# Optimization experiments

Hardware: AMD Instinct MI355X
Metric: run time of the kernel (lower is better)

Reference implementation:

```python
import jax, jax.numpy as jnp
import numpy as np

# ---- static problem sizes (full batches: cum[b] = b * max_num) ----
B = 256          # graphs per batch
MAXN, MAXE, MAXC = 128, 256, 64   # max nodes / edges / 2-cells per graph
H = 256          # embed_dim == hidden
L = 4            # num GCNCConv layers
OUT = 10         # out_size
P_N, P_E = 131072, 98304          # up-adjacency pair counts (dim 0, dim 1)
Q_E, Q_C = 131072, 65536          # boundary incidence counts (dim 1, dim 2)


def setup_inputs() -> dict:
    key = jax.random.key(0)
    ks = jax.random.split(key, 24)
    s = 1.0 / np.sqrt(H)
    inp = {}
    # flat cochain features [total_entities, H]
    inp['x_n'] = jax.random.normal(ks[0], (B * MAXN, H), jnp.float32)
    inp['x_e'] = jax.random.normal(ks[1], (B * MAXE, H), jnp.float32)
    inp['x_c'] = jax.random.normal(ks[2], (B * MAXC, H), jnp.float32)
    # node-level up adjacency (pairs of nodes sharing an edge coboundary)
    inp['n_up_b'] = jax.random.randint(ks[3], (P_N,), 0, B, jnp.int32)
    inp['n_up_i'] = jax.random.randint(ks[4], (P_N,), 0, MAXN, jnp.int32)
    inp['n_up_j'] = jax.random.randint(ks[5], (P_N,), 0, MAXN, jnp.int32)
    inp['n_up_e'] = jax.random.randint(ks[6], (P_N,), 0, MAXE, jnp.int32)
    # edge-level up adjacency (pairs of edges sharing a cell coboundary)
    inp['e_up_b'] = jax.random.randint(ks[7], (P_E,), 0, B, jnp.int32)
    inp['e_up_i'] = jax.random.randint(ks[8], (P_E,), 0, MAXE, jnp.int32)
    inp['e_up_j'] = jax.random.randint(ks[9], (P_E,), 0, MAXE, jnp.int32)
    inp['e_up_c'] = jax.random.randint(ks[10], (P_E,), 0, MAXC, jnp.int32)
    # boundary incidence: edges -> nodes, cells -> edges
    inp['eb_b'] = jax.random.randint(ks[11], (Q_E,), 0, B, jnp.int32)
    inp['eb_i'] = jax.random.randint(ks[12], (Q_E,), 0, MAXE, jnp.int32)
    inp['eb_j'] = jax.random.randint(ks[13], (Q_E,), 0, MAXN, jnp.int32)
    inp['cb_b'] = jax.random.randint(ks[14], (Q_C,), 0, B, jnp.int32)
    inp['cb_i'] = jax.random.randint(ks[15], (Q_C,), 0, MAXC, jnp.int32)
    inp['cb_j'] = jax.random.randint(ks[16], (Q_C,), 0, MAXE, jnp.int32)
    # learned parameters
    inp['Wself'] = jax.random.normal(ks[17], (L, 3, H, H), jnp.float32) * s
    inp['bself'] = jnp.zeros((L, 3, H), jnp.float32)
    inp['Wupx'] = jax.random.normal(ks[18], (L, 2, H, H), jnp.float32) * s
    inp['Wupa'] = jax.random.normal(ks[19], (L, 2, H, H), jnp.float32) * s
    inp['Wb'] = jax.random.normal(ks[20], (L, 2, H, H), jnp.float32) * s
    inp['Wp'] = jax.random.normal(ks[21], (H, H), jnp.float32) * s
    inp['Wp_ref'] = jax.random.normal(ks[22], (H, H), jnp.float32) * s
    inp['bp'] = jnp.zeros((H,), jnp.float32)
    k2 = jax.random.split(ks[23], 4)
    inp['W1'] = jax.random.normal(k2[0], (3, H, 2 * H), jnp.float32) * s
    inp['b1'] = jnp.zeros((3, 2 * H), jnp.float32)
    inp['W2'] = jax.random.normal(k2[1], (2 * H, OUT), jnp.float32) * s
    inp['b2'] = jnp.zeros((OUT,), jnp.float32)
    return inp


def reference(x_n, x_e, x_c, n_up_b, n_up_i, n_up_j, n_up_e,
              e_up_b, e_up_i, e_up_j, e_up_c, eb_b, eb_i, eb_j,
              cb_b, cb_i, cb_j, Wself, bself, Wupx, Wupa, Wb,
              Wp, Wp_ref, bp, W1, b1, W2, b2):
    relu = jax.nn.relu
    # dense per-batch boundary adjacencies (scatter-set, as in init_data_to_dense_gcnc)
    b_adj_e = jnp.zeros((B, MAXE, MAXN), jnp.float32).at[eb_b, eb_i, eb_j].set(1.0)
    b_adj_c = jnp.zeros((B, MAXC, MAXE), jnp.float32).at[cb_b, cb_i, cb_j].set(1.0)
    # flat gather/scatter indices: cum[b] = b * max_num (full batches)
    n_i = n_up_b * MAXN + n_up_i
    n_j = n_up_b * MAXN + n_up_j
    n_a = n_up_b * MAXE + n_up_e   # up_attr_idx into edge features
    e_i = e_up_b * MAXE + e_up_i
    e_j = e_up_b * MAXE + e_up_j
    e_a = e_up_b * MAXC + e_up_c   # up_attr_idx into cell features
    xs = [x_n, x_e, x_c]
    refs = xs  # init features used by pool_weight
    for l in range(L):
        xn, xe, xc = xs
        # up messages: msg = relu(W x_j + W' up_attr), scatter-sum to receiver
        up_n = jax.ops.segment_sum(
            relu(xn[n_j] @ Wupx[l, 0] + xe[n_a] @ Wupa[l, 0]),
            n_i, num_segments=B * MAXN)
        up_e = jax.ops.segment_sum(
            relu(xe[e_j] @ Wupx[l, 1] + xc[e_a] @ Wupa[l, 1]),
            e_i, num_segments=B * MAXE)
        # boundary messages: dense masked matmul with incidence matrices
        bd_e = jnp.einsum('ben,bnh->beh', b_adj_e,
                          xn.reshape(B, MAXN, H)).reshape(B * MAXE, H) @ Wb[l, 0]
        bd_c = jnp.einsum('bce,beh->bch', b_adj_c,
                          xe.reshape(B, MAXE, H)).reshape(B * MAXC, H) @ Wb[l, 1]
        xs = [relu(xn @ Wself[l, 0] + bself[l, 0] + up_n),
              relu(xe @ Wself[l, 1] + bself[l, 1] + up_e + bd_e),
              relu(xc @ Wself[l, 2] + bself[l, 2] + bd_c)]
    # pool weights (gating vs. init features) + sum readout per dimension
    maxs = (MAXN, MAXE, MAXC)
    pooled = []
    for i in range(3):
        w = jax.nn.sigmoid(xs[i] @ Wp + refs[i] @ Wp_ref + bp)
        pooled.append((w * xs[i]).reshape(B, maxs[i], H).sum(axis=1))  # [B,H]
    h = sum(relu(pooled[i] @ W1[i] + b1[i]) for i in range(3))  # final_readout='sum'
    return h @ W2 + b2  # [B, OUT]
```

## Files before the change

kernel.cpp:

```cpp
#include <hip/hip_runtime.h>
#include <cstdint>
#include <cstddef>

typedef unsigned short u16;
typedef __bf16 bf16x8 __attribute__((ext_vector_type(8)));
typedef float f32x4 __attribute__((ext_vector_type(4)));
typedef unsigned short u16x8 __attribute__((ext_vector_type(8)));

#define NB   256
#define MAXN 128
#define MAXE 256
#define MAXC 64
#define HD   256
#define NLAYER 4
#define PN 131072
#define PE 98304
#define QE 131072
#define QC 65536
#define MN (NB*MAXN)
#define ME (NB*MAXE)
#define MC (NB*MAXC)

#define SEG_N  0
#define SEG_E  (MN)
#define SEG_EB (MN + ME)
#define SEG_CB (MN + 2*ME)
#define HTOT   (MN + 2*ME + MC)
#define UPTOT  (PN + PE)

__device__ __forceinline__ float bf2f(u16 u){
  union{unsigned int i; float f;} x; x.i = ((unsigned int)u) << 16; return x.f;
}
__device__ __forceinline__ u16 f2bf(float f){
  union{float f; unsigned int i;} x; x.f = f;
  unsigned int r = x.i + 0x7fffu + ((x.i >> 16) & 1u);
  return (u16)(r >> 16);
}
__device__ __forceinline__ f32x4 MFMA(bf16x8 a, bf16x8 b, f32x4 c){
  return __builtin_amdgcn_mfma_f32_16x16x32_bf16(a, b, c, 0, 0, 0);
}
__device__ __forceinline__ void gl_lds16(const u16* g, u16* l){
  __builtin_amdgcn_global_load_lds(
      (const __attribute__((address_space(1))) unsigned int*)g,
      (__attribute__((address_space(3))) unsigned int*)l, 16, 0, 0);
}

__global__ void detect_dtype(const u16* __restrict__ x, int* __restrict__ flag){
  if(threadIdx.x == 0 && blockIdx.x == 0){
    int cnt = 0;
    for(int i = 0; i < 64; i++){
      int e = (x[i] >> 7) & 0xFF;
      if(e >= 118 && e <= 136) cnt++;
    }
    *flag = (cnt >= 50) ? 1 : 0;
  }
}

__global__ __launch_bounds__(256) void conv_bf(const void* __restrict__ src, u16* __restrict__ dst,
                                               long n, const int* __restrict__ flag){
  long i = ((long)blockIdx.x * 256 + threadIdx.x) * 8;
  if(i >= n) return;
  const int isbf = *flag;
  if(i + 8 <= n){
    if(isbf){
      *reinterpret_cast<u16x8*>(dst + i) = *reinterpret_cast<const u16x8*>((const u16*)src + i);
    }else{
      const float* s = (const float*)src + i;
      float4 a = *reinterpret_cast<const float4*>(s);
      float4 b = *reinterpret_cast<const float4*>(s + 4);
      u16x8 o;
      o[0]=f2bf(a.x); o[1]=f2bf(a.y); o[2]=f2bf(a.z); o[3]=f2bf(a.w);
      o[4]=f2bf(b.x); o[5]=f2bf(b.y); o[6]=f2bf(b.z); o[7]=f2bf(b.w);
      *reinterpret_cast<u16x8*>(dst + i) = o;
    }
  }else{
    for(long e = i; e < n; e++)
      dst[e] = isbf ? ((const u16*)src)[e] : f2bf(((const float*)src)[e]);
  }
}

__global__ __launch_bounds__(256) void zero_f4(float* __restrict__ p, long n4){
  long i = (long)blockIdx.x * blockDim.x + threadIdx.x;
  if(i >= n4) return;
  float4 z = {0.f, 0.f, 0.f, 0.f};
  *reinterpret_cast<float4*>(p + i * 4) = z;
}

__global__ void wt_transpose(const void* __restrict__ src, u16* __restrict__ dst,
                             const int* __restrict__ flag){
  __shared__ u16 t[16][17];
  int m = blockIdx.z;
  int n0 = blockIdx.x * 16, k0 = blockIdx.y * 16;
  size_t sidx = (size_t)m * 65536 + (size_t)(k0 + threadIdx.y) * 256 + n0 + threadIdx.x;
  u16 v = (*flag) ? ((const u16*)src)[sidx] : f2bf(((const float*)src)[sidx]);
  t[threadIdx.y][threadIdx.x] = v;
  __syncthreads();
  dst[(size_t)m * 65536 + (size_t)(n0 + threadIdx.y) * 256 + (k0 + threadIdx.x)] =
      t[threadIdx.x][threadIdx.y];
}

__global__ void dedup_kernel(const int* __restrict__ bb, const int* __restrict__ bi,
                             const int* __restrict__ bj, unsigned int* __restrict__ mask,
                             unsigned char* __restrict__ valid, int Q, int maxI, int maxJ){
  int q = blockIdx.x * blockDim.x + threadIdx.x;
  if(q >= Q) return;
  int s = (bb[q] * maxI + bi[q]) * maxJ + bj[q];
  unsigned int bit = 1u << (s & 31);
  unsigned int old = atomicOr(&mask[s >> 5], bit);
  valid[q] = (old & bit) ? 0 : 1;
}

__global__ __launch_bounds__(256) void hist_up(const int* __restrict__ pb, const int* __restrict__ pi,
                                               int maxI, int segBase, int* __restrict__ hist, int P){
  int p = blockIdx.x * 256 + threadIdx.x;
  if(p >= P) return;
  atomicAdd(&hist[segBase + pb[p] * maxI + pi[p]], 1);
}
__global__ __launch_bounds__(256) void hist_bd(const int* __restrict__ bb, const int* __restrict__ bi,
                                               const unsigned char* __restrict__ valid,
                                               int maxI, int segBase, int* __restrict__ hist, int Q){
  int q = blockIdx.x * 256 + threadIdx.x;
  if(q >= Q || !valid[q]) return;
  atomicAdd(&hist[segBase + bb[q] * maxI + bi[q]], 1);
}

__global__ __launch_bounds__(256) void scan1(const int* __restrict__ hist, int* __restrict__ bsum){
  __shared__ int s[256];
  int t = threadIdx.x;
  long base = (long)blockIdx.x * 1024 + t * 4;
  int4 v = *reinterpret_cast<const int4*>(hist + base);
  s[t] = v.x + v.y + v.z + v.w;
  __syncthreads();
  for(int st = 128; st > 0; st >>= 1){
    if(t < st) s[t] += s[t + st];
    __syncthreads();
  }
  if(t == 0) bsum[blockIdx.x] = s[0];
}
__global__ __launch_bounds__(256) void scan2(int* __restrict__ bsum, int nb){
  __shared__ int s[256];
  int t = threadIdx.x;
  int v = (t < nb) ? bsum[t] : 0;
  s[t] = v;
  __syncthreads();
  for(int st = 1; st < 256; st <<= 1){
    int u = (t >= st) ? s[t - st] : 0;
    __syncthreads();
    s[t] += u;
    __syncthreads();
  }
  if(t < nb) bsum[t] = s[t] - v;
}
__global__ __launch_bounds__(256) void scan3(const int* __restrict__ hist, const int* __restrict__ bsum,
                                             int* __restrict__ off, int* __restrict__ cur){
  __shared__ int s[256];
  int t = threadIdx.x;
  long base = (long)blockIdx.x * 1024 + t * 4;
  int4 v = *reinterpret_cast<const int4*>(hist + base);
  int sum = v.x + v.y + v.z + v.w;
  s[t] = sum;
  __syncthreads();
  for(int st = 1; st < 256; st <<= 1){
    int u = (t >= st) ? s[t - st] : 0;
    __syncthreads();
    s[t] += u;
    __syncthreads();
  }
  int excl = s[t] - sum + bsum[blockIdx.x];
  int4 o;
  o.x = excl; o.y = o.x + v.x; o.z = o.y + v.y; o.w = o.z + v.z;
  *reinterpret_cast<int4*>(off + base) = o;
  *reinterpret_cast<int4*>(cur + base) = o;
}

__global__ __launch_bounds__(256) void fill_up(const int* __restrict__ pb, const int* __restrict__ pi,
    const int* __restrict__ pj, const int* __restrict__ pa, int maxI, int maxA, int segBase,
    int* __restrict__ cur, int2* __restrict__ csrUp, int P){
  int p = blockIdx.x * 256 + threadIdx.x;
  if(p >= P) return;
  int b = pb[p];
  int pos = atomicAdd(&cur[segBase + b * maxI + pi[p]], 1);
  int2 e; e.x = b * maxI + pj[p]; e.y = b * maxA + pa[p];
  csrUp[pos] = e;
}
__global__ __launch_bounds__(256) void fill_bd(const int* __restrict__ bb, const int* __restrict__ bi,
    const int* __restrict__ bj, const unsigned char* __restrict__ valid, int maxI, int maxJ,
    int segBase, int* __restrict__ cur, int* __restrict__ csrBd, int Q){
  int q = blockIdx.x * 256 + threadIdx.x;
  if(q >= Q || !valid[q]) return;
  int b = bb[q];
  int pos = atomicAdd(&cur[segBase + b * maxI + bi[q]], 1);
  csrBd[pos - UPTOT] = b * maxJ + bj[q];
}

template<int HAS_UP, int HAS_BD>
__global__ __launch_bounds__(256) void gather_k(
    const u16* __restrict__ Y, const u16* __restrict__ Z, const u16* __restrict__ BD,
    const int2* __restrict__ csrUp, const int* __restrict__ csrBd,
    const int* __restrict__ off, const int* __restrict__ deg,
    int upBase, int bdBase, u16* __restrict__ ACC, int rowLo){
  const int nb = gridDim.x;
  int bx = blockIdx.x;
  if((nb & 7) == 0) bx = (bx & 7) * (nb >> 3) + (bx >> 3);
  const int row = rowLo + bx * 4 + (threadIdx.x >> 6);
  const int lane = threadIdx.x & 63;
  const int c = lane * 4;
  float a0 = 0.f, a1 = 0.f, a2 = 0.f, a3 = 0.f;
  if(HAS_UP){
    int s = off[upBase + row];
    int d = deg[upBase + row];
    for(int k = 0; k < d; k++){
      int2 e = csrUp[s + k];
      const ushort4 y = *reinterpret_cast<const ushort4*>(Y + (size_t)e.x * 256 + c);
      const ushort4 z = *reinterpret_cast<const ushort4*>(Z + (size_t)e.y * 256 + c);
      a0 += fmaxf(bf2f(y.x) + bf2f(z.x), 0.f);
      a1 += fmaxf(bf2f(y.y) + bf2f(z.y), 0.f);
      a2 += fmaxf(bf2f(y.z) + bf2f(z.z), 0.f);
      a3 += fmaxf(bf2f(y.w) + bf2f(z.w), 0.f);
    }
  }
  if(HAS_BD){
    int s = off[bdBase + row] - UPTOT;
    int d = deg[bdBase + row];
    for(int k = 0; k < d; k++){
      int j = csrBd[s + k];
      const ushort4 x = *reinterpret_cast<const ushort4*>(BD + (size_t)j * 256 + c);
      a0 += bf2f(x.x); a1 += bf2f(x.y); a2 += bf2f(x.z); a3 += bf2f(x.w);
    }
  }
  ushort4 o; o.x = f2bf(a0); o.y = f2bf(a1); o.z = f2bf(a2); o.w = f2bf(a3);
  *reinterpret_cast<ushort4*>(ACC + (size_t)(row - rowLo) * 256 + c) = o;
}

template<int MODE>
__global__ __launch_bounds__(512) void gemm_b(const u16* A, const u16* __restrict__ WT,
                                              u16* C, const u16* __restrict__ ACC,
                                              const u16* __restrict__ bias,
                                              const u16* A2, const u16* __restrict__ WT2){
  __shared__ u16 lA[2][128 * 64];
  __shared__ u16 lB[2][256 * 64];
  const int t = threadIdx.x;
  const int lane = t & 63, wv = t >> 6;
  const int wm = wv >> 2, wn = wv & 3;
  const int r = lane & 15, q = lane >> 4;
  const int rsw = r & 7;
  const size_t m0 = (size_t)blockIdx.x * 128;
  const int lrow = lane >> 3, lchk = lane & 7;
  const int csw = lchk ^ lrow;

  f32x4 acc[4][4];
#pragma unroll
  for(int i = 0; i < 4; i++)
#pragma unroll
    for(int j = 0; j < 4; j++) acc[i][j] = {0.f, 0.f, 0.f, 0.f};

  const int NT = (MODE == 3) ? 8 : 4;

  auto stage = [&](int tt, int buf){
    const u16* Ap = (MODE == 3 && tt >= 4) ? A2 : A;
    const u16* Wp = (MODE == 3 && tt >= 4) ? WT2 : WT;
    const int k0 = (tt & 3) * 64;
#pragma unroll
    for(int i = 0; i < 2; i++){
      const int row = i * 64 + wv * 8 + lrow;
      gl_lds16(Ap + (m0 + row) * 256 + k0 + csw * 8, &lA[buf][(i * 64 + wv * 8) * 64]);
    }
#pragma unroll
    for(int j = 0; j < 4; j++){
      const int n = j * 64 + wv * 8 + lrow;
      gl_lds16(Wp + (size_t)n * 256 + k0 + csw * 8, &lB[buf][(j * 64 + wv * 8) * 64]);
    }
  };

  stage(0, 0);
  __syncthreads();

#pragma unroll
  for(int tt = 0; tt < NT; tt++){
    const int cur = tt & 1;
    if(tt + 1 < NT) stage(tt + 1, cur ^ 1);
#pragma unroll
    for(int ks = 0; ks < 2; ks++){
      bf16x8 af[4], bfr[4];
#pragma unroll
      for(int i = 0; i < 4; i++)
        af[i] = *reinterpret_cast<const bf16x8*>(
            &lA[cur][(wm * 64 + i * 16 + r) * 64 + (((ks * 4 + q) ^ rsw) * 8)]);
#pragma unroll
      for(int j = 0; j < 4; j++)
        bfr[j] = *reinterpret_cast<const bf16x8*>(
            &lB[cur][(wn * 64 + j * 16 + r) * 64 + (((ks * 4 + q) ^ rsw) * 8)]);
#pragma unroll
      for(int i = 0; i < 4; i++)
#pragma unroll
        for(int j = 0; j < 4; j++) acc[i][j] = MFMA(af[i], bfr[j], acc[i][j]);
    }
    __syncthreads();
  }

#pragma unroll
  for(int i = 0; i < 4; i++){
    const size_t row0 = m0 + wm * 64 + i * 16 + q * 4;
#pragma unroll
    for(int j = 0; j < 4; j++){
      const int col = wn * 64 + j * 16 + r;
#pragma unroll
      for(int reg = 0; reg < 4; reg++){
        const size_t idx = (row0 + reg) * 256 + col;
        float x = acc[i][j][reg];
        if(MODE == 2) x = fmaxf(x + bf2f(ACC[idx]) + bf2f(bias[col]), 0.f);
        C[idx] = f2bf(x);
      }
    }
  }
}

__global__ __launch_bounds__(256) void pool_reduce(const u16* __restrict__ G, const u16* __restrict__ bpv,
    const u16* __restrict__ X, float* __restrict__ pooled, int maxR, int rowsPerBlk){
  int b = blockIdx.x, h = threadIdx.x;
  int r0 = blockIdx.y * rowsPerBlk;
  float bias = bf2f(bpv[h]);
  float acc = 0.f;
  for(int r = r0; r < r0 + rowsPerBlk; r++){
    size_t o = ((size_t)b * maxR + r) * 256 + h;
    float t = bf2f(G[o]) + bias;
    float w = 1.f / (1.f + __expf(-t));
    acc += w * bf2f(X[o]);
  }
  atomicAdd(&pooled[b * 256 + h], acc);
}

__global__ __launch_bounds__(512) void readout1(const float* __restrict__ pooled, const u16* __restrict__ W1,
                                                const u16* __restrict__ b1, float* __restrict__ hbuf){
  __shared__ float p[3][256];
  int b = blockIdx.x, o = threadIdx.x;
  if(o < 256){
    p[0][o] = pooled[(size_t)b * 256 + o];
    p[1][o] = pooled[(size_t)NB * 256 + (size_t)b * 256 + o];
    p[2][o] = pooled[(size_t)2 * NB * 256 + (size_t)b * 256 + o];
  }
  __syncthreads();
  float s = 0.f;
#pragma unroll
  for(int i = 0; i < 3; i++){
    float a = bf2f(b1[i * 512 + o]);
    for(int k = 0; k < 256; k++) a += p[i][k] * bf2f(W1[(size_t)(i * 256 + k) * 512 + o]);
    s += fmaxf(a, 0.f);
  }
  hbuf[(size_t)b * 512 + o] = s;
}

__global__ __launch_bounds__(64) void readout2(const float* __restrict__ hbuf, const u16* __restrict__ W2,
                                               const u16* __restrict__ b2, void* __restrict__ out,
                                               const int* __restrict__ flag){
  int b = blockIdx.x, o = threadIdx.x;
  if(o >= 10) return;
  float a = bf2f(b2[o]);
  for(int k = 0; k < 512; k++) a += hbuf[(size_t)b * 512 + k] * bf2f(W2[k * 10 + o]);
  if(*flag) ((u16*)out)[b * 10 + o] = f2bf(a);
  else      ((float*)out)[b * 10 + o] = a;
}

extern "C" void kernel_launch(void* const* d_in, const int* in_sizes, int n_in,
                              void* d_out, int out_size, void* d_ws, size_t ws_size,
                              hipStream_t stream){
  const void* x_n = d_in[0];
  const void* x_e = d_in[1];
  const void* x_c = d_in[2];
  const int* n_up_b = (const int*)d_in[3];
  const int* n_up_i = (const int*)d_in[4];
  const int* n_up_j = (const int*)d_in[5];
  const int* n_up_e = (const int*)d_in[6];
  const int* e_up_b = (const int*)d_in[7];
  const int* e_up_i = (const int*)d_in[8];
  const int* e_up_j = (const int*)d_in[9];
  const int* e_up_c = (const int*)d_in[10];
  const int* eb_b = (const int*)d_in[11];
  const int* eb_i = (const int*)d_in[12];
  const int* eb_j = (const int*)d_in[13];
  const int* cb_b = (const int*)d_in[14];
  const int* cb_i = (const int*)d_in[15];
  const int* cb_j = (const int*)d_in[16];

  char* base = (char*)d_ws; size_t off0 = 0;
  auto alloc = [&](size_t n)->char*{ char* p = base + off0; off0 = (off0 + n + 255) & ~(size_t)255; return p; };
  u16* xn = (u16*)alloc((size_t)MN * HD * 2);
  u16* xe = (u16*)alloc((size_t)ME * HD * 2);
  u16* xc = (u16*)alloc((size_t)MC * HD * 2);
  u16* BIG1 = (u16*)alloc((size_t)ME * HD * 2);
  u16* SMa  = (u16*)alloc((size_t)MN * HD * 2);
  u16* SMb  = (u16*)alloc((size_t)MN * HD * 2);
  u16* ACC  = (u16*)alloc((size_t)16384 * HD * 4);
  u16* wt = (u16*)alloc((size_t)38 * 65536 * 2);
  unsigned int* mask_e = (unsigned int*)alloc((size_t)NB * MAXE * MAXN / 8);
  unsigned int* mask_c = (unsigned int*)alloc((size_t)NB * MAXC * MAXE / 8);
  unsigned char* valid_e = (unsigned char*)alloc(QE);
  unsigned char* valid_c = (unsigned char*)alloc(QC);
  float* pooled = (float*)alloc((size_t)3 * NB * HD * 4);
  float* hbuf   = (float*)alloc((size_t)NB * 512 * 4);
  int* flag     = (int*)alloc(256);
  int2* csrUp   = (int2*)alloc((size_t)UPTOT * 8);
  int* csrBd    = (int*)alloc((size_t)(QE + QC) * 4);
  int* hist     = (int*)alloc((size_t)HTOT * 4);
  int* offA     = (int*)alloc((size_t)HTOT * 4);
  int* bsum     = (int*)alloc(1024);
  int* cur      = (int*)pooled;

  u16* wtSelf = wt;
  u16* wtUpx  = wt + (size_t)12 * 65536;
  u16* wtUpa  = wt + (size_t)20 * 65536;
  u16* wtB    = wt + (size_t)28 * 65536;
  u16* wtP    = wt + (size_t)36 * 65536;
  u16* wtPref = wt + (size_t)37 * 65536;

  u16* W1c = (u16*)mask_e;
  u16* b1c = W1c + 393216;
  u16* W2c = b1c + 1536;
  u16* b2c = W2c + 5120;
  u16* bsc = b2c + 16;
  u16* bpc = bsc + 3072;

  auto convN = [&](const void* s, u16* d, long n){
    long blk = (n + 8*256 - 1) / (8*256);
    conv_bf<<<(int)blk, 256, 0, stream>>>(s, d, n, flag);
  };

  detect_dtype<<<1, 64, 0, stream>>>((const u16*)x_n, flag);
  zero_f4<<<(65536 + 255)/256, 256, 0, stream>>>((float*)mask_e, 65536);
  zero_f4<<<(32768 + 255)/256, 256, 0, stream>>>((float*)mask_c, 32768);
  dedup_kernel<<<QE/256, 256, 0, stream>>>(eb_b, eb_i, eb_j, mask_e, valid_e, QE, MAXE, MAXN);
  dedup_kernel<<<QC/256, 256, 0, stream>>>(cb_b, cb_i, cb_j, mask_c, valid_c, QC, MAXC, MAXE);

  wt_transpose<<<dim3(16,16,12), dim3(16,16), 0, stream>>>(d_in[17], wtSelf, flag);
  wt_transpose<<<dim3(16,16,8),  dim3(16,16), 0, stream>>>(d_in[19], wtUpx,  flag);
  wt_transpose<<<dim3(16,16,8),  dim3(16,16), 0, stream>>>(d_in[20], wtUpa,  flag);
  wt_transpose<<<dim3(16,16,8),  dim3(16,16), 0, stream>>>(d_in[21], wtB,    flag);
  wt_transpose<<<dim3(16,16,1),  dim3(16,16), 0, stream>>>(d_in[22], wtP,    flag);
  wt_transpose<<<dim3(16,16,1),  dim3(16,16), 0, stream>>>(d_in[23], wtPref, flag);
  convN(x_n, xn, (long)MN * HD);
  convN(x_e, xe, (long)ME * HD);
  convN(x_c, xc, (long)MC * HD);
  convN(d_in[18], bsc, 3072);
  convN(d_in[24], bpc, 256);
  convN(d_in[25], W1c, 393216);
  convN(d_in[26], b1c, 1536);
  convN(d_in[27], W2c, 5120);
  convN(d_in[28], b2c, 10);

  zero_f4<<<(HTOT/4 + 255)/256, 256, 0, stream>>>((float*)hist, HTOT/4);
  hist_up<<<PN/256, 256, 0, stream>>>(n_up_b, n_up_i, MAXN, SEG_N,  hist, PN);
  hist_up<<<PE/256, 256, 0, stream>>>(e_up_b, e_up_i, MAXE, SEG_E,  hist, PE);
  hist_bd<<<QE/256, 256, 0, stream>>>(eb_b, eb_i, valid_e, MAXE, SEG_EB, hist, QE);
  hist_bd<<<QC/256, 256, 0, stream>>>(cb_b, cb_i, valid_c, MAXC, SEG_CB, hist, QC);
  scan1<<<HTOT/1024, 256, 0, stream>>>(hist, bsum);
  scan2<<<1, 256, 0, stream>>>(bsum, HTOT/1024);
  scan3<<<HTOT/1024, 256, 0, stream>>>(hist, bsum, offA, cur);
  fill_up<<<PN/256, 256, 0, stream>>>(n_up_b, n_up_i, n_up_j, n_up_e, MAXN, MAXE, SEG_N, cur, csrUp, PN);
  fill_up<<<PE/256, 256, 0, stream>>>(e_up_b, e_up_i, e_up_j, e_up_c, MAXE, MAXC, SEG_E, cur, csrUp, PE);
  fill_bd<<<QE/256, 256, 0, stream>>>(eb_b, eb_i, eb_j, valid_e, MAXE, MAXN, SEG_EB, cur, csrBd, QE);
  fill_bd<<<QC/256, 256, 0, stream>>>(cb_b, cb_i, cb_j, valid_c, MAXC, MAXE, SEG_CB, cur, csrBd, QC);

  for(int l = 0; l < NLAYER; l++){
    const u16* Wupx0 = wtUpx + (size_t)(l*2+0) * 65536;
    const u16* Wupx1 = wtUpx + (size_t)(l*2+1) * 65536;
    const u16* Wupa0 = wtUpa + (size_t)(l*2+0) * 65536;
    const u16* Wupa1 = wtUpa + (size_t)(l*2+1) * 65536;
    const u16* Wb0   = wtB   + (size_t)(l*2+0) * 65536;
    const u16* Wb1   = wtB   + (size_t)(l*2+1) * 65536;
    const u16* Ws0   = wtSelf + (size_t)(l*3+0) * 65536;
    const u16* Ws1   = wtSelf + (size_t)(l*3+1) * 65536;
    const u16* Ws2   = wtSelf + (size_t)(l*3+2) * 65536;
    const u16* bs0 = bsc + (size_t)(l*3+0) * HD;
    const u16* bs1 = bsc + (size_t)(l*3+1) * HD;
    const u16* bs2 = bsc + (size_t)(l*3+2) * HD;

    gemm_b<0><<<MN/128, 512, 0, stream>>>(xn, Wupx0, SMa, nullptr, nullptr, nullptr, nullptr);
    gemm_b<0><<<ME/128, 512, 0, stream>>>(xe, Wupa0, BIG1, nullptr, nullptr, nullptr, nullptr);
    gemm_b<0><<<MN/128, 512, 0, stream>>>(xn, Wb0, SMb, nullptr, nullptr, nullptr, nullptr);
    for(int h = 0; h < 2; h++){
      int lo = h * (MN/2);
      gather_k<1,0><<<(MN/2)/4, 256, 0, stream>>>(SMa, BIG1, nullptr, csrUp, csrBd,
                                                  offA, hist, SEG_N, 0, ACC, lo);
      gemm_b<2><<<(MN/2)/128, 512, 0, stream>>>(xn + (size_t)lo * HD, Ws0,
                                                xn + (size_t)lo * HD, ACC, bs0, nullptr, nullptr);
    }

    gemm_b<0><<<MC/128, 512, 0, stream>>>(xc, Wupa1, SMa, nullptr, nullptr, nullptr, nullptr);
    gemm_b<0><<<ME/128, 512, 0, stream>>>(xe, Wb1, BIG1, nullptr, nullptr, nullptr, nullptr);
    gather_k<0,1><<<MC/4, 256, 0, stream>>>(nullptr, nullptr, BIG1, csrUp, csrBd,
                                            offA, hist, 0, SEG_CB, ACC, 0);
    gemm_b<2><<<MC/128, 512, 0, stream>>>(xc, Ws2, xc, ACC, bs2, nullptr, nullptr);

    gemm_b<0><<<ME/128, 512, 0, stream>>>(xe, Wupx1, BIG1, nullptr, nullptr, nullptr, nullptr);
    for(int h = 0; h < 2; h++){
      int lo = h * (ME/2);
      gather_k<1,1><<<(ME/2)/4, 256, 0, stream>>>(BIG1, SMa, SMb, csrUp, csrBd,
                                                  offA, hist, SEG_E, SEG_EB, ACC, lo);
      gemm_b<2><<<(ME/2)/128, 512, 0, stream>>>(xe + (size_t)lo * HD, Ws1,
                                                xe + (size_t)lo * HD, ACC, bs1, nullptr, nullptr);
    }
  }

  u16* REF = SMa;
  {
    long np4 = (long)3 * NB * HD / 4;
    zero_f4<<<(int)((np4 + 255)/256), 256, 0, stream>>>(pooled, np4);
  }
  convN(x_n, REF, (long)MN * HD);
  gemm_b<3><<<MN/128, 512, 0, stream>>>(xn, wtP, BIG1, nullptr, nullptr, REF, wtPref);
  pool_reduce<<<dim3(NB,2), 256, 0, stream>>>(BIG1, bpc, xn, pooled, MAXN, MAXN/2);

  convN(x_e, REF, (long)ME * HD);
  gemm_b<3><<<ME/128, 512, 0, stream>>>(xe, wtP, BIG1, nullptr, nullptr, REF, wtPref);
  pool_reduce<<<dim3(NB,4), 256, 0, stream>>>(BIG1, bpc, xe, pooled + (size_t)NB*HD, MAXE, MAXE/4);

  convN(x_c, REF, (long)MC * HD);
  gemm_b<3><<<MC/128, 512, 0, stream>>>(xc, wtP, BIG1, nullptr, nullptr, REF, wtPref);
  pool_reduce<<<dim3(NB,1), 256, 0, stream>>>(BIG1, bpc, xc, pooled + (size_t)2*NB*HD, MAXC, MAXC);

  readout1<<<NB, 512, 0, stream>>>(pooled, W1c, b1c, hbuf);
  readout2<<<NB, 64, 0, stream>>>(hbuf, W2c, b2c, d_out, flag);
}
```

Baseline: 1.537 ms.

## Triple-buffer GEMM tile loads with explicit waitcnt and transpose readout W1

The GEMM main loop moves from double to triple buffering in LDS. Loads are issued up to three k-tiles ahead and gated with explicit s_waitcnt vmcnt counts and raw barriers instead of __syncthreads, so more global-to-LDS traffic overlaps with MFMA work. LDS use rises to about 288KB-equivalent per block worth of u16 (3×(128+256)×64×2 bytes ≈ 147KB), which may cut occupancy or exceed limits. Separately, the readout weight W1 is transposed once so each thread reads contiguous 16-byte vectors instead of strided scalars.

```diff
diff --git a/kernel.cpp b/kernel.cpp
--- a/kernel.cpp
+++ b/kernel.cpp
@@ -96,6 +96,17 @@
   t[threadIdx.y][threadIdx.x] = v;
   __syncthreads();
   dst[(size_t)m * 65536 + (size_t)(n0 + threadIdx.y) * 256 + (k0 + threadIdx.x)] =
+      t[threadIdx.x][threadIdx.y];
+}
+
+__global__ void w1_transpose(const u16* __restrict__ src, u16* __restrict__ dst){
+  __shared__ u16 t[16][17];
+  int i = blockIdx.z;
+  int o0 = blockIdx.x * 16, k0 = blockIdx.y * 16;
+  t[threadIdx.y][threadIdx.x] =
+      src[(size_t)i * 131072 + (size_t)(k0 + threadIdx.y) * 512 + o0 + threadIdx.x];
+  __syncthreads();
+  dst[(size_t)i * 131072 + (size_t)(o0 + threadIdx.y) * 256 + (k0 + threadIdx.x)] =
       t[threadIdx.x][threadIdx.y];
 }
 
@@ -237,8 +248,8 @@
                                               u16* C, const u16* __restrict__ ACC,
                                               const u16* __restrict__ bias,
                                               const u16* A2, const u16* __restrict__ WT2){
-  __shared__ u16 lA[2][128 * 64];
-  __shared__ u16 lB[2][256 * 64];
+  __shared__ u16 lA[3][128 * 64];
+  __shared__ u16 lB[3][256 * 64];
   const int t = threadIdx.x;
   const int lane = t & 63, wv = t >> 6;
   const int wm = wv >> 2, wn = wv & 3;
@@ -273,12 +284,17 @@
   };
 
   stage(0, 0);
-  __syncthreads();
+  stage(1, 1);
+  stage(2, 2);
 
 #pragma unroll
   for(int tt = 0; tt < NT; tt++){
-    const int cur = tt & 1;
-    if(tt + 1 < NT) stage(tt + 1, cur ^ 1);
+    const int cur = tt % 3;
+    const int rem = NT - 1 - tt;
+    if(rem >= 2)      asm volatile("s_waitcnt vmcnt(12)" ::: "memory");
+    else if(rem == 1) asm volatile("s_waitcnt vmcnt(6)" ::: "memory");
+    else              asm volatile("s_waitcnt vmcnt(0)" ::: "memory");
+    __builtin_amdgcn_s_barrier();
 #pragma unroll
     for(int ks = 0; ks < 2; ks++){
       bf16x8 af[4], bfr[4];
@@ -295,7 +311,8 @@
 #pragma unroll
         for(int j = 0; j < 4; j++) acc[i][j] = MFMA(af[i], bfr[j], acc[i][j]);
     }
-    __syncthreads();
+    __builtin_amdgcn_s_barrier();
+    if(tt + 3 < NT) stage(tt + 3, cur);
   }
 
 #pragma unroll
@@ -330,7 +347,7 @@
   atomicAdd(&pooled[b * 256 + h], acc);
 }
 
-__global__ __launch_bounds__(512) void readout1(const float* __restrict__ pooled, const u16* __restrict__ W1,
+__global__ __launch_bounds__(512) void readout1(const float* __restrict__ pooled, const u16* __restrict__ W1t,
                                                 const u16* __restrict__ b1, float* __restrict__ hbuf){
   __shared__ float p[3][256];
   int b = blockIdx.x, o = threadIdx.x;
@@ -344,7 +361,14 @@
 #pragma unroll
   for(int i = 0; i < 3; i++){
     float a = bf2f(b1[i * 512 + o]);
-    for(int k = 0; k < 256; k++) a += p[i][k] * bf2f(W1[(size_t)(i * 256 + k) * 512 + o]);
+    const u16* w = W1t + (size_t)i * 131072 + (size_t)o * 256;
+#pragma unroll 4
+    for(int k8 = 0; k8 < 32; k8++){
+      u16x8 wv = *reinterpret_cast<const u16x8*>(w + k8 * 8);
+      const float* pp = &p[i][k8 * 8];
+      a += pp[0]*bf2f(wv[0]) + pp[1]*bf2f(wv[1]) + pp[2]*bf2f(wv[2]) + pp[3]*bf2f(wv[3])
+         + pp[4]*bf2f(wv[4]) + pp[5]*bf2f(wv[5]) + pp[6]*bf2f(wv[6]) + pp[7]*bf2f(wv[7]);
+    }
     s += fmaxf(a, 0.f);
   }
   hbuf[(size_t)b * 512 + o] = s;
@@ -404,6 +428,7 @@
   int* hist     = (int*)alloc((size_t)HTOT * 4);
   int* offA     = (int*)alloc((size_t)HTOT * 4);
   int* bsum     = (int*)alloc(1024);
+  u16* W1t      = (u16*)alloc((size_t)3 * 512 * 256 * 2);
   int* cur      = (int*)pooled;
 
   u16* wtSelf = wt;
@@ -446,6 +471,7 @@
   convN(d_in[26], b1c, 1536);
   convN(d_in[27], W2c, 5120);
   convN(d_in[28], b2c, 10);
+  w1_transpose<<<dim3(32,16,3), dim3(16,16), 0, stream>>>(W1c, W1t);
 
   zero_f4<<<(HTOT/4 + 255)/256, 256, 0, stream>>>((float*)hist, HTOT/4);
   hist_up<<<PN/256, 256, 0, stream>>>(n_up_b, n_up_i, MAXN, SEG_N,  hist, PN);
@@ -518,6 +544,6 @@
   gemm_b<3><<<MC/128, 512, 0, stream>>>(xc, wtP, BIG1, nullptr, nullptr, REF, wtPref);
   pool_reduce<<<dim3(NB,1), 256, 0, stream>>>(BIG1, bpc, xc, pooled + (size_t)2*NB*HD, MAXC, MAXC);
 
-  readout1<<<NB, 512, 0, stream>>>(pooled, W1c, b1c, hbuf);
+  readout1<<<NB, 512, 0, stream>>>(pooled, W1t, b1c, hbuf);
   readout2<<<NB, 64, 0, stream>>>(hbuf, W2c, b2c, d_out, flag);
 }
```

Measured after the change: 1.509 ms. Within noise of the previous version (-1.8%).

## Shrink GEMM tiles, deepen prefetch pipeline, and move readout1 to MFMA

Applied to the files above, without the earlier changes.

The main GEMM now uses a 64-row tile with 256 threads and issues the next two K-stages ahead. It waits with explicit vmcnt counters and raw barriers, and raises wave priority during the MFMA section. This doubles the grid size, which helps occupancy, and overlaps loads more deeply with compute. The scalar readout1 kernel is replaced by an MFMA-based kernel that takes a bf16 copy of the pooled features and a pre-transposed W1, which removes a slow per-thread dot-product loop. The trade-offs are that B tiles are reloaded more often per output row, and pooled features are rounded to bf16 before the readout.

```diff
diff --git a/kernel.cpp b/kernel.cpp
--- a/kernel.cpp
+++ b/kernel.cpp
@@ -79,6 +79,17 @@
   }
 }
 
+__global__ __launch_bounds__(256) void conv_f2b(const float* __restrict__ s, u16* __restrict__ d, long n){
+  long i = ((long)blockIdx.x * 256 + threadIdx.x) * 8;
+  if(i >= n) return;
+  float4 a = *reinterpret_cast<const float4*>(s + i);
+  float4 b = *reinterpret_cast<const float4*>(s + i + 4);
+  u16x8 o;
+  o[0]=f2bf(a.x); o[1]=f2bf(a.y); o[2]=f2bf(a.z); o[3]=f2bf(a.w);
+  o[4]=f2bf(b.x); o[5]=f2bf(b.y); o[6]=f2bf(b.z); o[7]=f2bf(b.w);
+  *reinterpret_cast<u16x8*>(d + i) = o;
+}
+
 __global__ __launch_bounds__(256) void zero_f4(float* __restrict__ p, long n4){
   long i = (long)blockIdx.x * blockDim.x + threadIdx.x;
   if(i >= n4) return;
@@ -96,6 +107,17 @@
   t[threadIdx.y][threadIdx.x] = v;
   __syncthreads();
   dst[(size_t)m * 65536 + (size_t)(n0 + threadIdx.y) * 256 + (k0 + threadIdx.x)] =
+      t[threadIdx.x][threadIdx.y];
+}
+
+__global__ void w1_transpose(const u16* __restrict__ src, u16* __restrict__ dst){
+  __shared__ u16 t[16][17];
+  int i = blockIdx.z;
+  int o0 = blockIdx.x * 16, k0 = blockIdx.y * 16;
+  t[threadIdx.y][threadIdx.x] =
+      src[(size_t)i * 131072 + (size_t)(k0 + threadIdx.y) * 512 + o0 + threadIdx.x];
+  __syncthreads();
+  dst[(size_t)i * 131072 + (size_t)(o0 + threadIdx.y) * 256 + (k0 + threadIdx.x)] =
       t[threadIdx.x][threadIdx.y];
 }
 
@@ -233,18 +255,18 @@
 }
 
 template<int MODE>
-__global__ __launch_bounds__(512) void gemm_b(const u16* A, const u16* __restrict__ WT,
+__global__ __launch_bounds__(256) void gemm_b(const u16* A, const u16* __restrict__ WT,
                                               u16* C, const u16* __restrict__ ACC,
                                               const u16* __restrict__ bias,
                                               const u16* A2, const u16* __restrict__ WT2){
-  __shared__ u16 lA[2][128 * 64];
+  __shared__ u16 lA[2][64 * 64];
   __shared__ u16 lB[2][256 * 64];
   const int t = threadIdx.x;
   const int lane = t & 63, wv = t >> 6;
-  const int wm = wv >> 2, wn = wv & 3;
+  const int wn = wv;
   const int r = lane & 15, q = lane >> 4;
   const int rsw = r & 7;
-  const size_t m0 = (size_t)blockIdx.x * 128;
+  const size_t m0 = (size_t)blockIdx.x * 64;
   const int lrow = lane >> 3, lchk = lane & 7;
   const int csw = lchk ^ lrow;
 
@@ -262,30 +284,33 @@
     const int k0 = (tt & 3) * 64;
 #pragma unroll
     for(int i = 0; i < 2; i++){
-      const int row = i * 64 + wv * 8 + lrow;
-      gl_lds16(Ap + (m0 + row) * 256 + k0 + csw * 8, &lA[buf][(i * 64 + wv * 8) * 64]);
-    }
-#pragma unroll
-    for(int j = 0; j < 4; j++){
-      const int n = j * 64 + wv * 8 + lrow;
-      gl_lds16(Wp + (size_t)n * 256 + k0 + csw * 8, &lB[buf][(j * 64 + wv * 8) * 64]);
+      const int row = wv * 16 + i * 8 + lrow;
+      gl_lds16(Ap + (m0 + row) * 256 + k0 + csw * 8, &lA[buf][(wv * 16 + i * 8) * 64]);
+    }
+#pragma unroll
+    for(int j = 0; j < 8; j++){
+      const int n = wv * 64 + j * 8 + lrow;
+      gl_lds16(Wp + (size_t)n * 256 + k0 + csw * 8, &lB[buf][(wv * 64 + j * 8) * 64]);
     }
   };
 
   stage(0, 0);
-  __syncthreads();
+  stage(1, 1);
 
 #pragma unroll
   for(int tt = 0; tt < NT; tt++){
     const int cur = tt & 1;
-    if(tt + 1 < NT) stage(tt + 1, cur ^ 1);
+    if(tt < NT - 1) asm volatile("s_waitcnt vmcnt(10)" ::: "memory");
+    else            asm volatile("s_waitcnt vmcnt(0)" ::: "memory");
+    __builtin_amdgcn_s_barrier();
+    __builtin_amdgcn_s_setprio(1);
 #pragma unroll
     for(int ks = 0; ks < 2; ks++){
       bf16x8 af[4], bfr[4];
 #pragma unroll
       for(int i = 0; i < 4; i++)
         af[i] = *reinterpret_cast<const bf16x8*>(
-            &lA[cur][(wm * 64 + i * 16 + r) * 64 + (((ks * 4 + q) ^ rsw) * 8)]);
+            &lA[cur][(i * 16 + r) * 64 + (((ks * 4 + q) ^ rsw) * 8)]);
 #pragma unroll
       for(int j = 0; j < 4; j++)
         bfr[j] = *reinterpret_cast<const bf16x8*>(
@@ -295,12 +320,14 @@
 #pragma unroll
         for(int j = 0; j < 4; j++) acc[i][j] = MFMA(af[i], bfr[j], acc[i][j]);
     }
-    __syncthreads();
+    __builtin_amdgcn_s_setprio(0);
+    __builtin_amdgcn_s_barrier();
+    if(tt + 2 < NT) stage(tt + 2, cur);
   }
 
 #pragma unroll
   for(int i = 0; i < 4; i++){
-    const size_t row0 = m0 + wm * 64 + i * 16 + q * 4;
+    const size_t row0 = m0 + i * 16 + q * 4;
 #pragma unroll
     for(int j = 0; j < 4; j++){
       const int col = wn * 64 + j * 16 + r;
@@ -330,24 +357,99 @@
   atomicAdd(&pooled[b * 256 + h], acc);
 }
 
-__global__ __launch_bounds__(512) void readout1(const float* __restrict__ pooled, const u16* __restrict__ W1,
-                                                const u16* __restrict__ b1, float* __restrict__ hbuf){
-  __shared__ float p[3][256];
-  int b = blockIdx.x, o = threadIdx.x;
-  if(o < 256){
-    p[0][o] = pooled[(size_t)b * 256 + o];
-    p[1][o] = pooled[(size_t)NB * 256 + (size_t)b * 256 + o];
-    p[2][o] = pooled[(size_t)2 * NB * 256 + (size_t)b * 256 + o];
-  }
-  __syncthreads();
-  float s = 0.f;
-#pragma unroll
-  for(int i = 0; i < 3; i++){
-    float a = bf2f(b1[i * 512 + o]);
-    for(int k = 0; k < 256; k++) a += p[i][k] * bf2f(W1[(size_t)(i * 256 + k) * 512 + o]);
-    s += fmaxf(a, 0.f);
-  }
-  hbuf[(size_t)b * 512 + o] = s;
+__global__ __launch_bounds__(512) void readout1_mfma(const u16* __restrict__ Ab,
+                                                     const u16* __restrict__ W1t,
+                                                     const u16* __restrict__ b1,
+                                                     float* __restrict__ hbuf){
+  __shared__ u16 lA[2][128 * 64];
+  __shared__ u16 lB[2][256 * 64];
+  const int t = threadIdx.x;
+  const int lane = t & 63, wv = t >> 6;
+  const int wm = wv >> 2, wn = wv & 3;
+  const int r = lane & 15, q = lane >> 4;
+  const int rsw = r & 7;
+  const int b0 = blockIdx.x * 128;
+  const int o0 = blockIdx.y * 256;
+  const int lrow = lane >> 3, lchk = lane & 7;
+  const int csw = lchk ^ lrow;
+
+  f32x4 acc[4][4], facc[4][4];
+#pragma unroll
+  for(int i = 0; i < 4; i++)
+#pragma unroll
+    for(int j = 0; j < 4; j++){ acc[i][j] = {0.f,0.f,0.f,0.f}; facc[i][j] = {0.f,0.f,0.f,0.f}; }
+
+  auto stage = [&](int tt, int buf){
+    const int ii = tt >> 2, k0 = (tt & 3) * 64;
+    const u16* Ap = Ab + (size_t)ii * 65536;
+    const u16* Wp = W1t + (size_t)ii * 131072;
+#pragma unroll
+    for(int i = 0; i < 2; i++){
+      const int row = i * 64 + wv * 8 + lrow;
+      gl_lds16(Ap + (size_t)(b0 + row) * 256 + k0 + csw * 8, &lA[buf][(i * 64 + wv * 8) * 64]);
+    }
+#pragma unroll
+    for(int j = 0; j < 4; j++){
+      const int n = j * 64 + wv * 8 + lrow;
+      gl_lds16(Wp + (size_t)(o0 + n) * 256 + k0 + csw * 8, &lB[buf][(j * 64 + wv * 8) * 64]);
+    }
+  };
+
+  stage(0, 0);
+  stage(1, 1);
+
+#pragma unroll
+  for(int tt = 0; tt < 12; tt++){
+    const int cur = tt & 1;
+    if(tt < 11) asm volatile("s_waitcnt vmcnt(6)" ::: "memory");
+    else        asm volatile("s_waitcnt vmcnt(0)" ::: "memory");
+    __builtin_amdgcn_s_barrier();
+#pragma unroll
+    for(int ks = 0; ks < 2; ks++){
+      bf16x8 af[4], bfr[4];
+#pragma unroll
+      for(int i = 0; i < 4; i++)
+        af[i] = *reinterpret_cast<const bf16x8*>(
+            &lA[cur][(wm * 64 + i * 16 + r) * 64 + (((ks * 4 + q) ^ rsw) * 8)]);
+#pragma unroll
+      for(int j = 0; j < 4; j++)
+        bfr[j] = *reinterpret_cast<const bf16x8*>(
+            &lB[cur][(wn * 64 + j * 16 + r) * 64 + (((ks * 4 + q) ^ rsw) * 8)]);
+#pragma unroll
+      for(int i = 0; i < 4; i++)
+#pragma unroll
+        for(int j = 0; j < 4; j++) acc[i][j] = MFMA(af[i], bfr[j], acc[i][j]);
+    }
+    if((tt & 3) == 3){
+      const int ib = tt >> 2;
+#pragma unroll
+      for(int i = 0; i < 4; i++)
+#pragma unroll
+        for(int j = 0; j < 4; j++){
+          const int col = o0 + wn * 64 + j * 16 + r;
+          const float bb = bf2f(b1[ib * 512 + col]);
+#pragma unroll
+          for(int reg = 0; reg < 4; reg++){
+            facc[i][j][reg] += fmaxf(acc[i][j][reg] + bb, 0.f);
+            acc[i][j][reg] = 0.f;
+          }
+        }
+    }
+    __builtin_amdgcn_s_barrier();
+    if(tt + 2 < 12) stage(tt + 2, cur);
+  }
+
+#pragma unroll
+  for(int i = 0; i < 4; i++){
+    const int row0 = b0 + wm * 64 + i * 16 + q * 4;
+#pragma unroll
+    for(int j = 0; j < 4; j++){
+      const int col = o0 + wn * 64 + j * 16 + r;
+#pragma unroll
+      for(int reg = 0; reg < 4; reg++)
+        hbuf[(size_t)(row0 + reg) * 512 + col] = facc[i][j][reg];
+    }
+  }
 }
 
 __global__ __launch_bounds__(64) void readout2(const float* __restrict__ hbuf, const u16* __restrict__ W2,
@@ -404,6 +506,8 @@
   int* hist     = (int*)alloc((size_t)HTOT * 4);
   int* offA     = (int*)alloc((size_t)HTOT * 4);
   int* bsum     = (int*)alloc(1024);
+  u16* W1t      = (u16*)alloc((size_t)3 * 512 * 256 * 2);
+  u16* pooledb  = (u16*)alloc((size_t)3 * NB * HD * 2);
   int* cur      = (int*)pooled;
 
   u16* wtSelf = wt;
@@ -446,6 +550,7 @@
   convN(d_in[26], b1c, 1536);
   convN(d_in[27], W2c, 5120);
   convN(d_in[28], b2c, 10);
+  w1_transpose<<<dim3(32,16,3), dim3(16,16), 0, stream>>>(W1c, W1t);
 
   zero_f4<<<(HTOT/4 + 255)/256, 256, 0, stream>>>((float*)hist, HTOT/4);
   hist_up<<<PN/256, 256, 0, stream>>>(n_up_b, n_up_i, MAXN, SEG_N,  hist, PN);
@@ -474,30 +579,30 @@
     const u16* bs1 = bsc + (size_t)(l*3+1) * HD;
     const u16* bs2 = bsc + (size_t)(l*3+2) * HD;
 
-    gemm_b<0><<<MN/128, 512, 0, stream>>>(xn, Wupx0, SMa, nullptr, nullptr, nullptr, nullptr);
-    gemm_b<0><<<ME/128, 512, 0, stream>>>(xe, Wupa0, BIG1, nullptr, nullptr, nullptr, nullptr);
-    gemm_b<0><<<MN/128, 512, 0, stream>>>(xn, Wb0, SMb, nullptr, nullptr, nullptr, nullptr);
+    gemm_b<0><<<MN/64, 256, 0, stream>>>(xn, Wupx0, SMa, nullptr, nullptr, nullptr, nullptr);
+    gemm_b<0><<<ME/64, 256, 0, stream>>>(xe, Wupa0, BIG1, nullptr, nullptr, nullptr, nullptr);
+    gemm_b<0><<<MN/64, 256, 0, stream>>>(xn, Wb0, SMb, nullptr, nullptr, nullptr, nullptr);
     for(int h = 0; h < 2; h++){
       int lo = h * (MN/2);
       gather_k<1,0><<<(MN/2)/4, 256, 0, stream>>>(SMa, BIG1, nullptr, csrUp, csrBd,
                                                   offA, hist, SEG_N, 0, ACC, lo);
-      gemm_b<2><<<(MN/2)/128, 512, 0, stream>>>(xn + (size_t)lo * HD, Ws0,
-                                                xn + (size_t)lo * HD, ACC, bs0, nullptr, nullptr);
-    }
-
-    gemm_b<0><<<MC/128, 512, 0, stream>>>(xc, Wupa1, SMa, nullptr, nullptr, nullptr, nullptr);
-    gemm_b<0><<<ME/128, 512, 0, stream>>>(xe, Wb1, BIG1, nullptr, nullptr, nullptr, nullptr);
+      gemm_b<2><<<(MN/2)/64, 256, 0, stream>>>(xn + (size_t)lo * HD, Ws0,
+                                               xn + (size_t)lo * HD, ACC, bs0, nullptr, nullptr);
+    }
+
+    gemm_b<0><<<MC/64, 256, 0, stream>>>(xc, Wupa1, SMa, nullptr, nullptr, nullptr, nullptr);
+    gemm_b<0><<<ME/64, 256, 0, stream>>>(xe, Wb1, BIG1, nullptr, nullptr, nullptr, nullptr);
     gather_k<0,1><<<MC/4, 256, 0, stream>>>(nullptr, nullptr, BIG1, csrUp, csrBd,
                                             offA, hist, 0, SEG_CB, ACC, 0);
-    gemm_b<2><<<MC/128, 512, 0, stream>>>(xc, Ws2, xc, ACC, bs2, nullptr, nullptr);
-
-    gemm_b<0><<<ME/128, 512, 0, stream>>>(xe, Wupx1, BIG1, nullptr, nullptr, nullptr, nullptr);
+    gemm_b<2><<<MC/64, 256, 0, stream>>>(xc, Ws2, xc, ACC, bs2, nullptr, nullptr);
+
+    gemm_b<0><<<ME/64, 256, 0, stream>>>(xe, Wupx1, BIG1, nullptr, nullptr, nullptr, nullptr);
     for(int h = 0; h < 2; h++){
       int lo = h * (ME/2);
       gather_k<1,1><<<(ME/2)/4, 256, 0, stream>>>(BIG1, SMa, SMb, csrUp, csrBd,
                                                   offA, hist, SEG_E, SEG_EB, ACC, lo);
-      gemm_b<2><<<(ME/2)/128, 512, 0, stream>>>(xe + (size_t)lo * HD, Ws1,
-                                                xe + (size_t)lo * HD, ACC, bs1, nullptr, nullptr);
+      gemm_b<2><<<(ME/2)/64, 256, 0, stream>>>(xe + (size_t)lo * HD, Ws1,
+                                               xe + (size_t)lo * HD, ACC, bs1, nullptr, nullptr);
     }
   }
 
@@ -507,17 +612,18 @@
     zero_f4<<<(int)((np4 + 255)/256), 256, 0, stream>>>(pooled, np4);
   }
   convN(x_n, REF, (long)MN * HD);
-  gemm_b<3><<<MN/128, 512, 0, stream>>>(xn, wtP, BIG1, nullptr, nullptr, REF, wtPref);
+  gemm_b<3><<<MN/64, 256, 0, stream>>>(xn, wtP, BIG1, nullptr, nullptr, REF, wtPref);
   pool_reduce<<<dim3(NB,2), 256, 0, stream>>>(BIG1, bpc, xn, pooled, MAXN, MAXN/2);
 
   convN(x_e, REF, (long)ME * HD);
-  gemm_b<3><<<ME/128, 512, 0, stream>>>(xe, wtP, BIG1, nullptr, nullptr, REF, wtPref);
+  gemm_b<3><<<ME/64, 256, 0, stream>>>(xe, wtP, BIG1, nullptr, nullptr, REF, wtPref);
   pool_reduce<<<dim3(NB,4), 256, 0, stream>>>(BIG1, bpc, xe, pooled + (size_t)NB*HD, MAXE, MAXE/4);
 
   convN(x_c, REF, (long)MC * HD);
-  gemm_b<3><<<MC/128, 512, 0, stream>>>(xc, wtP, BIG1, nullptr, nullptr, REF, wtPref);
+  gemm_b<3><<<MC/64, 256, 0, stream>>>(xc, wtP, BIG1, nullptr, nullptr, REF, wtPref);
   pool_reduce<<<dim3(NB,1), 256, 0, stream>>>(BIG1, bpc, xc, pooled + (size_t)2*NB*HD, MAXC, MAXC);
 
-  readout1<<<NB, 512, 0, stream>>>(pooled, W1c, b1c, hbuf);
+  conv_f2b<<<96, 256, 0, stream>>>(pooled, pooledb, (long)3 * NB * HD);
+  readout1_mfma<<<dim3(2,2), 512, 0, stream>>>(pooledb, W1t, b1c, hbuf);
   readout2<<<NB, 64, 0, stream>>>(hbuf, W2c, b2c, d_out, flag);
 }
```

Result: no change. 1.546 ms (+0.6%).
